# Optimization experiments

Measured on AMD Instinct MI355X. Metric: run time of the kernel, lower is better.

## Reference

```python
import jax, jax.numpy as jnp
import numpy as np
import math

DIM = 1024
HEADS = 16
DHEAD = 64
WINDOW = 512
STRIDE = 32


def setup_inputs() -> dict:
    key = jax.random.key(0)
    ks = jax.random.split(key, 4)
    x = jax.random.normal(ks[0], (2, 4096, DIM), dtype=jnp.float32)
    W_qkv = jax.random.normal(ks[1], (DIM, 3 * HEADS * DHEAD), dtype=jnp.float32) * 0.02
    W_gate = jax.random.normal(ks[2], (DIM, 1), dtype=jnp.float32) * 0.02
    b_gate = jnp.zeros((1,), dtype=jnp.float32)
    W_out = jax.random.normal(ks[3], (HEADS * DHEAD, DIM), dtype=jnp.float32) * 0.02
    b_out = jnp.zeros((DIM,), dtype=jnp.float32)
    return {"x": x, "W_qkv": W_qkv, "W_gate": W_gate, "b_gate": b_gate,
            "W_out": W_out, "b_out": b_out}


def _local_attention(q, k, v):
    # q,k,v: [b, s, h, d]; overlapping windows: query block W attends K/V block [i-W/2, i+W+W/2)
    b, s, h, d = q.shape
    W = WINDOW
    half = W // 2
    nW = s // W
    scale = 1.0 / math.sqrt(d)
    k_pad = jnp.pad(k, ((0, 0), (half, half), (0, 0), (0, 0)))
    v_pad = jnp.pad(v, ((0, 0), (half, half), (0, 0), (0, 0)))
    # gather each window's 2W-wide K/V block
    idx = jnp.arange(nW)[:, None] * W + jnp.arange(2 * W)[None, :]  # [nW, 2W]
    kb = k_pad[:, idx]  # [b, nW, 2W, h, d]
    vb = v_pad[:, idx]
    qb = q.reshape(b, nW, W, h, d)
    scores = jnp.einsum('bnwhd,bnthd->bnwht', qb, kb) * scale  # [b,nW,W,h,2W]
    valid = (idx >= half) & (idx < s + half)  # mask out zero padding at edges
    scores = jnp.where(valid[None, :, None, None, :], scores, jnp.float32(-1e9))
    attn = jax.nn.softmax(scores, axis=-1)
    out = jnp.einsum('bnwht,bnthd->bnwhd', attn, vb)
    return out.reshape(b, s, h, d)


def _sparse_global_attention(q, k, v):
    b, s, h, d = q.shape
    scale = 1.0 / math.sqrt(d)
    k_str = k[:, ::STRIDE]  # [b, s/STRIDE, h, d]
    v_str = v[:, ::STRIDE]
    scores = jnp.einsum('bshd,bthd->bsht', q, k_str) * scale
    attn = jax.nn.softmax(scores, axis=-1)
    return jnp.einsum('bsht,bthd->bshd', attn, v_str)


def reference(x, W_qkv, W_gate, b_gate, W_out, b_out):
    b, s, dim = x.shape
    qkv = x @ W_qkv  # [b, s, 3*h*d]
    q, k, v = jnp.split(qkv, 3, axis=-1)
    q = q.reshape(b, s, HEADS, DHEAD)
    k = k.reshape(b, s, HEADS, DHEAD)
    v = v.reshape(b, s, HEADS, DHEAD)
    local_out = _local_attention(q, k, v)
    global_out = _sparse_global_attention(q, k, v)
    combine = jax.nn.sigmoid(x @ W_gate + b_gate)  # [b, s, 1]
    gate = combine[..., None]  # [b, s, 1, 1] broadcasts over heads, dim_head
    out = gate * local_out + (1.0 - gate) * global_out
    out = out.reshape(b, s, HEADS * DHEAD)
    return out @ W_out + b_out
```

## Files before the change

### kernel.cpp

```cpp
#include <hip/hip_runtime.h>
#include <hip/hip_bf16.h>
#include <cstdint>
#include <cstddef>

typedef __attribute__((ext_vector_type(8))) short bfrag;
typedef __attribute__((ext_vector_type(4))) short short4v;
typedef __attribute__((ext_vector_type(4))) float facc;

static __device__ __forceinline__ short f2bf(float f) {
  __hip_bfloat16 h = __float2bfloat16(f);
  return *reinterpret_cast<short*>(&h);
}
static __device__ __forceinline__ float bf2f(short s) {
  union { float f; unsigned int u; } c; c.u = ((unsigned int)(unsigned short)s) << 16;
  return c.f;
}

static __device__ __forceinline__ void gload16(const short* g, short* l) {
  __builtin_amdgcn_global_load_lds(
      (const __attribute__((address_space(1))) unsigned int*)(g),
      (__attribute__((address_space(3))) unsigned int*)(l), 16, 0, 0);
}

#define SL 0.18033688011112043f

__global__ __launch_bounds__(256) void cvt_rows_gate(
    const float* __restrict__ src, short* __restrict__ dst,
    const float* __restrict__ Wg, const float* __restrict__ bg,
    float* __restrict__ g) {
  const int t = threadIdx.x;
  size_t i = (size_t)blockIdx.x * 256 + t;
  const facc* s4 = (const facc*)src;
  facc v0 = s4[i * 2], v1 = s4[i * 2 + 1];
  bfrag o;
  o[0] = f2bf(v0[0]); o[1] = f2bf(v0[1]); o[2] = f2bf(v0[2]); o[3] = f2bf(v0[3]);
  o[4] = f2bf(v1[0]); o[5] = f2bf(v1[1]); o[6] = f2bf(v1[2]); o[7] = f2bf(v1[3]);
  *(bfrag*)(dst + i * 8) = o;
  const facc* wr = (const facc*)(Wg + (t & 127) * 8);
  facc w0 = wr[0], w1 = wr[1];
  float s = v0[0]*w0[0] + v0[1]*w0[1] + v0[2]*w0[2] + v0[3]*w0[3]
          + v1[0]*w1[0] + v1[1]*w1[1] + v1[2]*w1[2] + v1[3]*w1[3];
  #pragma unroll
  for (int mm = 1; mm < 64; mm <<= 1) s += __shfl_xor(s, mm);
  __shared__ float gsum[4];
  if ((t & 63) == 0) gsum[t >> 6] = s;
  __syncthreads();
  if ((t & 127) == 0) {
    int half = t >> 7;
    float tot = gsum[half * 2] + gsum[half * 2 + 1] + bg[0];
    g[blockIdx.x * 2 + half] = 1.f / (1.f + __expf(-tot));
  }
}

__global__ __launch_bounds__(256) void cvt_T2(
    const float* __restrict__ s1, short* __restrict__ d1,
    const float* __restrict__ s2, short* __restrict__ d2) {
  __shared__ short tile[64][65];
  const int bx = blockIdx.x;
  const float* src; short* dst; int N; int n0;
  if (bx < 48) { src = s1; dst = d1; N = 3072; n0 = bx * 64; }
  else         { src = s2; dst = d2; N = 1024; n0 = (bx - 48) * 64; }
  int k0 = blockIdx.y * 64;
  int tx = threadIdx.x & 63, ty = threadIdx.x >> 6;
  #pragma unroll
  for (int i = ty; i < 64; i += 4)
    tile[i][tx] = f2bf(src[(size_t)(k0 + i) * N + n0 + tx]);
  __syncthreads();
  #pragma unroll
  for (int i = ty; i < 64; i += 4)
    dst[(size_t)(n0 + i) * 1024 + k0 + tx] = tile[tx][i];
}

__global__ __launch_bounds__(256) void prep_attn(
    const short* __restrict__ kb, const short* __restrict__ vb,
    short* __restrict__ vbt, short* __restrict__ vgt, short* __restrict__ kgs) {
  __shared__ short tile[64][65];
  const int t = threadIdx.x, tx = t & 63, ty = t >> 6;
  const int k0 = blockIdx.x * 64, bh = blockIdx.y;
  const size_t base = (size_t)bh * 262144;
  #pragma unroll
  for (int i = ty; i < 64; i += 4)
    tile[i][tx] = vb[base + (size_t)(k0 + i) * 64 + tx];
  __syncthreads();
  #pragma unroll
  for (int i = ty; i < 64; i += 4)
    vbt[base + (size_t)i * 4096 + k0 + tx] = tile[tx][i];
  if (t < 128) {
    int sk = t >> 6, d = t & 63;
    int gi = (k0 >> 5) + sk;
    vgt[(size_t)bh * 8192 + d * 128 + gi] = tile[sk * 32][d];
    kgs[(size_t)bh * 8192 + gi * 64 + d] = kb[base + (size_t)(k0 + sk * 32) * 64 + d];
  }
}

template <int EPI>
__global__ __launch_bounds__(256) void gemm_bt(
    const short* __restrict__ A, const short* __restrict__ Bt,
    int M, int N, int K,
    short* __restrict__ q_out, short* __restrict__ k_out, short* __restrict__ v_out,
    float* __restrict__ out, const float* __restrict__ bias) {
  __shared__ short Ab[2][128 * 32];
  __shared__ short Bb[2][128 * 32];
  const int t = threadIdx.x;
  const int l = t & 63;
  const int tile_m = blockIdx.y * 128;
  const int tile_n = blockIdx.x * 128;
  const int w = t >> 6;
  const int wm = (w >> 1) * 64, wn = (w & 1) * 64;
  const int c0 = t, c1 = t + 256;

  facc acc[4][4];
  #pragma unroll
  for (int i = 0; i < 4; ++i)
    #pragma unroll
    for (int j = 0; j < 4; ++j) acc[i][j] = (facc){0.f, 0.f, 0.f, 0.f};

  const short* Abase = A + (size_t)tile_m * K;
  const short* Bbase = Bt + (size_t)tile_n * K;
  const size_t ga0 = (size_t)(c0 >> 2) * K + (c0 & 3) * 8;
  const size_t ga1 = (size_t)(c1 >> 2) * K + (c1 & 3) * 8;

  auto stage = [&](int k0, int buf) {
    gload16(Abase + ga0 + k0, &Ab[buf][c0 * 8]);
    gload16(Abase + ga1 + k0, &Ab[buf][c1 * 8]);
    gload16(Bbase + ga0 + k0, &Bb[buf][c0 * 8]);
    gload16(Bbase + ga1 + k0, &Bb[buf][c1 * 8]);
  };

  stage(0, 0);
  __syncthreads();
  int buf = 0;
  for (int k0 = 0; k0 < K; k0 += 32) {
    if (k0 + 32 < K) stage(k0 + 32, buf ^ 1);
    bfrag af[4], bf[4];
    #pragma unroll
    for (int i = 0; i < 4; ++i)
      af[i] = *(const bfrag*)&Ab[buf][(wm + i * 16 + (l & 15)) * 32 + ((l >> 4) << 3)];
    #pragma unroll
    for (int i = 0; i < 4; ++i)
      bf[i] = *(const bfrag*)&Bb[buf][(wn + i * 16 + (l & 15)) * 32 + ((l >> 4) << 3)];
    #pragma unroll
    for (int mt = 0; mt < 4; ++mt)
      #pragma unroll
      for (int nt = 0; nt < 4; ++nt)
        acc[mt][nt] = __builtin_amdgcn_mfma_f32_16x16x32_bf16(af[mt], bf[nt], acc[mt][nt], 0, 0, 0);
    __syncthreads();
    buf ^= 1;
  }

  #pragma unroll
  for (int mt = 0; mt < 4; ++mt)
    #pragma unroll
    for (int nt = 0; nt < 4; ++nt) {
      int col = tile_n + wn + nt * 16 + (l & 15);
      int row0 = tile_m + wm + mt * 16 + ((l >> 4) << 2);
      if (EPI == 0) {
        int which = col >> 10, rem = col & 1023, hh = rem >> 6, dd = rem & 63;
        short* dst = (which == 0) ? q_out : ((which == 1) ? k_out : v_out);
        float vsc = (which == 0) ? SL : 1.f;
        #pragma unroll
        for (int r = 0; r < 4; ++r) {
          int m = row0 + r, b = m >> 12, s = m & 4095;
          dst[(((size_t)b * 16 + hh) * 4096 + s) * 64 + dd] = f2bf(acc[mt][nt][r] * vsc);
        }
      } else {
        float bv = bias[col];
        #pragma unroll
        for (int r = 0; r < 4; ++r)
          out[(size_t)(row0 + r) * N + col] = acc[mt][nt][r] + bv;
      }
    }
}


__global__ __launch_bounds__(512) void attn_fused(
    const short* __restrict__ qg, const short* __restrict__ kg,
    const short* __restrict__ vbt, const short* __restrict__ vgt,
    const short* __restrict__ kgs,
    const float* __restrict__ gate, short* __restrict__ comb) {
  __shared__ short Kt[2][64 * 64];
  __shared__ short Vt[2][64 * 64];
  __shared__ short Pb[8][16 * 64];

  const int t = threadIdx.x, l = t & 63, w = t >> 6;
  const int bid = blockIdx.x;
  const int yy = bid >> 3;
  const int bh = (bid & 7) * 4 + (yy >> 5);
  const int qblk = yy & 31;
  const int q0 = qblk * 128;
  const int b = bh >> 4, h = bh & 15;
  const int lo = l & 15, hi = l >> 4, hi4 = (l >> 4) << 2;

  const int n = q0 >> 9;
  int kstart = n * 512 - 256; if (kstart < 0) kstart = 0;
  int kend = n * 512 + 768; if (kend > 4096) kend = 4096;
  const int nloc = (kend - kstart) >> 6;

  const size_t qrow = (size_t)bh * 4096 + q0 + w * 16;
  bfrag qf[2];
  #pragma unroll
  for (int hf = 0; hf < 2; ++hf)
    qf[hf] = *(const bfrag*)(qg + (qrow + lo) * 64 + hf * 32 + hi * 8);

  bfrag ones;
  #pragma unroll
  for (int i = 0; i < 8; ++i) ones[i] = (short)0x3F80;

  facc ls_l = (facc){0.f, 0.f, 0.f, 0.f};
  facc ls_g = (facc){0.f, 0.f, 0.f, 0.f};
  facc o_l[4], o_g[4];
  #pragma unroll
  for (int nt = 0; nt < 4; ++nt) {
    o_l[nt] = (facc){0.f, 0.f, 0.f, 0.f};
    o_g[nt] = (facc){0.f, 0.f, 0.f, 0.f};
  }

  const int c = t, r = c >> 3;
  const int sl = (c & 7) ^ ((r & 7) ^ (r >> 3));

  const size_t kBaseL = (size_t)bh * 262144;
  const size_t sBase  = (size_t)bh * 8192;

  auto stageLoc = [&](int itl, int buf) {
    const int col = kstart + itl * 64;
    gload16(kg  + kBaseL + (size_t)(col + r) * 64 + sl * 8, &Kt[buf][c * 8]);
    gload16(vbt + kBaseL + (size_t)r * 4096 + col + sl * 8, &Vt[buf][c * 8]);
  };
  auto stageGlb = [&](int itg, int buf) {
    gload16(kgs + sBase + (size_t)(itg * 64 + r) * 64 + sl * 8, &Kt[buf][c * 8]);
    gload16(vgt + sBase + (size_t)r * 128 + itg * 64 + sl * 8, &Vt[buf][c * 8]);
  };

  const int gq = (lo & 7) ^ (lo >> 3);
  auto computeTile = [&](int buf, facc& ls, facc (&oacc)[4]) {
    bfrag kf[4][2];
    #pragma unroll
    for (int kt = 0; kt < 4; ++kt) {
      int key = kt * 16 + lo; int gk2 = (key & 7) ^ (key >> 3);
      const short* Kr = &Kt[buf][key * 64];
      kf[kt][0] = *(const bfrag*)&Kr[(hi * 8) ^ (gk2 << 3)];
      kf[kt][1] = *(const bfrag*)&Kr[(32 + hi * 8) ^ (gk2 << 3)];
    }
    bfrag vf[4][2];
    #pragma unroll
    for (int nt = 0; nt < 4; ++nt) {
      int d = nt * 16 + lo; int gd = (d & 7) ^ (d >> 3);
      const short* Vr = &Vt[buf][d * 64];
      vf[nt][0] = *(const bfrag*)&Vr[(hi * 8) ^ (gd << 3)];
      vf[nt][1] = *(const bfrag*)&Vr[(32 + hi * 8) ^ (gd << 3)];
    }
    short* Pw = &Pb[w][0];
    facc sA[4];
    #pragma unroll
    for (int kt = 0; kt < 4; ++kt) {
      facc z = (facc){0.f, 0.f, 0.f, 0.f};
      z = __builtin_amdgcn_mfma_f32_16x16x32_bf16(kf[kt][0], qf[0], z, 0, 0, 0);
      z = __builtin_amdgcn_mfma_f32_16x16x32_bf16(kf[kt][1], qf[1], z, 0, 0, 0);
      sA[kt] = z;
    }
    short4v pk[4];
    #pragma unroll
    for (int kt = 0; kt < 4; ++kt)
      #pragma unroll
      for (int rr = 0; rr < 4; ++rr)
        pk[kt][rr] = f2bf(exp2f(sA[kt][rr]));
    #pragma unroll
    for (int kt = 0; kt < 4; ++kt)
      *(short4v*)&Pw[lo * 64 + ((kt * 16 + hi4) ^ (gq << 3))] = pk[kt];
    bfrag pf0 = *(const bfrag*)&Pw[lo * 64 + ((hi * 8) ^ (gq << 3))];
    bfrag pf1 = *(const bfrag*)&Pw[lo * 64 + ((32 + hi * 8) ^ (gq << 3))];
    ls = __builtin_amdgcn_mfma_f32_16x16x32_bf16(pf0, ones, ls, 0, 0, 0);
    ls = __builtin_amdgcn_mfma_f32_16x16x32_bf16(pf1, ones, ls, 0, 0, 0);
    #pragma unroll
    for (int nt = 0; nt < 4; ++nt) {
      facc oo = oacc[nt];
      oo = __builtin_amdgcn_mfma_f32_16x16x32_bf16(pf0, vf[nt][0], oo, 0, 0, 0);
      oo = __builtin_amdgcn_mfma_f32_16x16x32_bf16(pf1, vf[nt][1], oo, 0, 0, 0);
      oacc[nt] = oo;
    }
  };

  stageGlb(0, 0);
  __syncthreads();
  stageGlb(1, 1);
  computeTile(0, ls_g, o_g);
  __syncthreads();
  stageLoc(0, 0);
  computeTile(1, ls_g, o_g);

  unsigned ogp[8];
  {
    float inv[4];
    #pragma unroll
    for (int rr = 0; rr < 4; ++rr) inv[rr] = 1.f / ls_g[rr];
    #pragma unroll
    for (int nt = 0; nt < 4; ++nt)
      #pragma unroll
      for (int rp = 0; rp < 2; ++rp) {
        unsigned a = (unsigned short)f2bf(o_g[nt][rp * 2] * inv[rp * 2]);
        unsigned bq = (unsigned short)f2bf(o_g[nt][rp * 2 + 1] * inv[rp * 2 + 1]);
        ogp[nt * 2 + rp] = a | (bq << 16);
      }
  }
  __syncthreads();

  int buf = 0;
  for (int itl = 0; itl < nloc; ++itl) {
    if (itl + 1 < nloc) stageLoc(itl + 1, buf ^ 1);
    computeTile(buf, ls_l, o_l);
    __syncthreads();
    buf ^= 1;
  }

  #pragma unroll
  for (int rr = 0; rr < 4; ++rr) {
    float invl = 1.f / ls_l[rr];
    int q = q0 + w * 16 + hi4 + rr;
    float gg = gate[b * 4096 + q];
    size_t obase = ((size_t)b * 4096 + q) * 1024 + h * 64;
    #pragma unroll
    for (int nt = 0; nt < 4; ++nt) {
      unsigned pw = ogp[nt * 2 + (rr >> 1)];
      float og = bf2f((short)((rr & 1) ? (pw >> 16) : (pw & 0xffff)));
      float val = gg * o_l[nt][rr] * invl + (1.f - gg) * og;
      comb[obase + nt * 16 + lo] = f2bf(val);
    }
  }
}

extern "C" void kernel_launch(void* const* d_in, const int* in_sizes, int n_in,
                              void* d_out, int out_size, void* d_ws, size_t ws_size,
                              hipStream_t stream) {
  const float* x    = (const float*)d_in[0];
  const float* Wqkv = (const float*)d_in[1];
  const float* Wg   = (const float*)d_in[2];
  const float* bg   = (const float*)d_in[3];
  const float* Wout = (const float*)d_in[4];
  const float* bout = (const float*)d_in[5];
  float* out = (float*)d_out;

  char* p = (char*)d_ws;
  short* xbf   = (short*)p; p += (size_t)8192 * 1024 * 2;
  short* WqkvT = (short*)p; p += (size_t)3072 * 1024 * 2;
  short* WoutT = (short*)p; p += (size_t)1024 * 1024 * 2;
  short* qb    = (short*)p; p += (size_t)32 * 4096 * 64 * 2;
  short* kb    = (short*)p; p += (size_t)32 * 4096 * 64 * 2;
  short* vb    = (short*)p; p += (size_t)32 * 4096 * 64 * 2;
  float* g     = (float*)p; p += (size_t)8192 * 4;
  short* vbt   = (short*)p; p += (size_t)32 * 64 * 4096 * 2;
  short* comb  = xbf;
  short* vgt   = WqkvT;
  short* kgs   = WqkvT + (size_t)32 * 64 * 128;

  cvt_rows_gate<<<4096, 256, 0, stream>>>(x, xbf, Wg, bg, g);
  cvt_T2<<<dim3(64, 16), 256, 0, stream>>>(Wqkv, WqkvT, Wout, WoutT);
  gemm_bt<0><<<dim3(24, 64), 256, 0, stream>>>(xbf, WqkvT, 8192, 3072, 1024,
                                               qb, kb, vb, nullptr, nullptr);
  prep_attn<<<dim3(64, 32), 256, 0, stream>>>(kb, vb, vbt, vgt, kgs);
  attn_fused<<<1024, 512, 0, stream>>>(qb, kb, vbt, vgt, kgs, g, comb);
  gemm_bt<1><<<dim3(8, 64), 256, 0, stream>>>(comb, WoutT, 8192, 1024, 1024,
                                              nullptr, nullptr, nullptr, out, bout);
}
```

Measured before the change: 274.1 us.

## Load K/V fragments directly from global memory instead of staging through LDS

Removes the double-buffered LDS staging of K and V tiles and their barriers. Each wave now reads its MFMA fragments straight from global memory, relying on L2/cache reuse across the 8 waves that share the same tiles. This drops the __syncthreads and LDS traffic, but each wave issues redundant global loads and no longer prefetches the next tile, so memory latency is exposed.

```diff
diff --git a/kernel.cpp b/kernel.cpp
--- a/kernel.cpp
+++ b/kernel.cpp
@@ -178,8 +178,6 @@
     const short* __restrict__ vbt, const short* __restrict__ vgt,
     const short* __restrict__ kgs,
     const float* __restrict__ gate, short* __restrict__ comb) {
-  __shared__ short Kt[2][64 * 64];
-  __shared__ short Vt[2][64 * 64];
   __shared__ short Pb[8][16 * 64];
 
   const int t = threadIdx.x, l = t & 63, w = t >> 6;
@@ -215,40 +213,23 @@
     o_g[nt] = (facc){0.f, 0.f, 0.f, 0.f};
   }
 
-  const int c = t, r = c >> 3;
-  const int sl = (c & 7) ^ ((r & 7) ^ (r >> 3));
-
   const size_t kBaseL = (size_t)bh * 262144;
   const size_t sBase  = (size_t)bh * 8192;
-
-  auto stageLoc = [&](int itl, int buf) {
-    const int col = kstart + itl * 64;
-    gload16(kg  + kBaseL + (size_t)(col + r) * 64 + sl * 8, &Kt[buf][c * 8]);
-    gload16(vbt + kBaseL + (size_t)r * 4096 + col + sl * 8, &Vt[buf][c * 8]);
-  };
-  auto stageGlb = [&](int itg, int buf) {
-    gload16(kgs + sBase + (size_t)(itg * 64 + r) * 64 + sl * 8, &Kt[buf][c * 8]);
-    gload16(vgt + sBase + (size_t)r * 128 + itg * 64 + sl * 8, &Vt[buf][c * 8]);
-  };
-
   const int gq = (lo & 7) ^ (lo >> 3);
-  auto computeTile = [&](int buf, facc& ls, facc (&oacc)[4]) {
-    bfrag kf[4][2];
-    #pragma unroll
-    for (int kt = 0; kt < 4; ++kt) {
-      int key = kt * 16 + lo; int gk2 = (key & 7) ^ (key >> 3);
-      const short* Kr = &Kt[buf][key * 64];
-      kf[kt][0] = *(const bfrag*)&Kr[(hi * 8) ^ (gk2 << 3)];
-      kf[kt][1] = *(const bfrag*)&Kr[(32 + hi * 8) ^ (gk2 << 3)];
-    }
-    bfrag vf[4][2];
-    #pragma unroll
-    for (int nt = 0; nt < 4; ++nt) {
-      int d = nt * 16 + lo; int gd = (d & 7) ^ (d >> 3);
-      const short* Vr = &Vt[buf][d * 64];
-      vf[nt][0] = *(const bfrag*)&Vr[(hi * 8) ^ (gd << 3)];
-      vf[nt][1] = *(const bfrag*)&Vr[(32 + hi * 8) ^ (gd << 3)];
-    }
+
+  auto computeTile = [&](const short* kB, const short* vB, int vStride,
+                         facc& ls, facc (&oacc)[4]) {
+    bfrag kf[4][2], vf[4][2];
+    #pragma unroll
+    for (int kt = 0; kt < 4; ++kt)
+      #pragma unroll
+      for (int hf = 0; hf < 2; ++hf)
+        kf[kt][hf] = *(const bfrag*)(kB + (size_t)(kt * 16 + lo) * 64 + hf * 32 + hi * 8);
+    #pragma unroll
+    for (int nt = 0; nt < 4; ++nt)
+      #pragma unroll
+      for (int hf = 0; hf < 2; ++hf)
+        vf[nt][hf] = *(const bfrag*)(vB + (size_t)(nt * 16 + lo) * vStride + hf * 32 + hi * 8);
     short* Pw = &Pb[w][0];
     facc sA[4];
     #pragma unroll
@@ -280,13 +261,10 @@
     }
   };
 
-  stageGlb(0, 0);
-  __syncthreads();
-  stageGlb(1, 1);
-  computeTile(0, ls_g, o_g);
-  __syncthreads();
-  stageLoc(0, 0);
-  computeTile(1, ls_g, o_g);
+  #pragma unroll
+  for (int itg = 0; itg < 2; ++itg)
+    computeTile(kgs + sBase + (size_t)itg * 64 * 64,
+                vgt + sBase + itg * 64, 128, ls_g, o_g);
 
   unsigned ogp[8];
   {
@@ -302,14 +280,11 @@
         ogp[nt * 2 + rp] = a | (bq << 16);
       }
   }
-  __syncthreads();
-
-  int buf = 0;
+
   for (int itl = 0; itl < nloc; ++itl) {
-    if (itl + 1 < nloc) stageLoc(itl + 1, buf ^ 1);
-    computeTile(buf, ls_l, o_l);
-    __syncthreads();
-    buf ^= 1;
+    const int col = kstart + itl * 64;
+    computeTile(kg + kBaseL + (size_t)col * 64,
+                vbt + kBaseL + col, 4096, ls_l, o_l);
   }
 
   #pragma unroll
```

After: 457.1 us. +66.8%, slower.
